# Kernel optimization log

Measured on AMD Instinct MI355X. Metric: run time of the kernel, lower is better.

Reference implementation:

```python
import jax, jax.numpy as jnp
import numpy as np

K = 32
START = K - 2  # index of <START>
STOP = K - 1   # index of <STOP>
NEG = -10000.0
B, T = 512, 2048


def setup_inputs() -> dict:
    key = jax.random.key(0)
    k1, k2, k3, k4 = jax.random.split(key, 4)
    feats = jax.random.normal(k1, (B, T, K), dtype=jnp.float32)
    transitions = jax.random.normal(k2, (K, K), dtype=jnp.float32)
    # constraints set in __init__: never transition TO START, never FROM STOP
    transitions = transitions.at[START, :].set(NEG).at[:, STOP].set(NEG)
    tags = jax.random.randint(k3, (B, T), 0, K - 2)          # real tags only
    lens = jnp.maximum(jax.random.randint(k4, (B,), 0, T), 1)  # at least 1 token
    return {"feats": feats, "transitions": transitions, "tags": tags, "lens": lens}


def _crf_loss(feats, transitions, tags, lens):
    Bn, Tn, Kn = feats.shape
    # ---- forward algorithm (log-partition) ----
    init = jnp.full((Bn, Kn), NEG, feats.dtype).at[:, START].set(0.0)

    def step(alpha, emit):
        # alpha[b,prev] + trans[next,prev] -> logsumexp over prev, then + emit[b,next]
        nxt = jax.scipy.special.logsumexp(
            alpha[:, None, :] + transitions[None, :, :], axis=2) + emit
        return nxt, nxt

    _, alphas = jax.lax.scan(step, init, jnp.swapaxes(feats, 0, 1))  # [T,B,K]
    alphas = jnp.concatenate([init[None], alphas], axis=0)           # [T+1,B,K]
    alpha_at_len = alphas[lens, jnp.arange(Bn)]                      # [B,K]
    forward_score = jax.scipy.special.logsumexp(
        alpha_at_len + transitions[STOP][None, :], axis=1)           # [B]

    # ---- gold score ----
    tags_stop = jnp.where(jnp.arange(Tn)[None, :] < lens[:, None], tags, STOP)
    pad_start = jnp.concatenate(
        [jnp.full((Bn, 1), START, tags.dtype), tags], axis=1)        # [B,T+1]
    pad_stop = jnp.concatenate(
        [tags_stop, jnp.full((Bn, 1), STOP, tags.dtype)], axis=1)    # [B,T+1]
    trans_mask = jnp.arange(Tn + 1)[None, :] <= lens[:, None]        # len+1 transitions
    trans_sc = jnp.where(trans_mask, transitions[pad_stop, pad_start], 0.0).sum(axis=1)
    emit_mask = jnp.arange(Tn)[None, :] < lens[:, None]
    emit_sc = jnp.where(
        emit_mask,
        jnp.take_along_axis(feats, tags[:, :, None], axis=2)[..., 0],
        0.0).sum(axis=1)
    gold_score = trans_sc + emit_sc

    return jnp.mean(forward_score - gold_score)


def reference(feats, transitions, tags, lens):
    return _crf_loss(feats, transitions, tags, lens)
```

## Files before the change

### kernel.cpp

```cpp
#include <hip/hip_runtime.h>
#include <cstdint>
#include <cstddef>

#define Kn 32
#define Bn 512
#define Tn 2048
#define CH 128
#define NC (Tn / CH)
#define GP 4
#define MMB (Bn * (NC / 4))
#define GB  Bn
#define START 30
#define STOP 31
#define LN2F 0.69314718055994530942f
#define QS 16
#define QF (QS * Kn)

typedef __attribute__((ext_vector_type(8))) short bf16x8;
typedef __attribute__((ext_vector_type(16))) float f32x16;
typedef __attribute__((ext_vector_type(2))) float f32x2;

union BF8 { bf16x8 v; unsigned u[4]; };

__device__ __forceinline__ unsigned pk2z(float lo, float hi) {
  return __builtin_amdgcn_perm(__float_as_uint(hi), __float_as_uint(lo),
                               0x07060302u);
}

__device__ __forceinline__ float bcast32(float v, int idx) {
  return __shfl(v, idx, 32);
}

__device__ __forceinline__ void plswap(unsigned& a, unsigned& b) {
  asm("v_permlane32_swap_b32 %0, %1" : "+v"(a), "+v"(b));
}

__global__ __launch_bounds__(256, 6) void crf_fused(
    const float* __restrict__ feats, const float* __restrict__ trans,
    const int* __restrict__ tags, const int* __restrict__ lens,
    float* __restrict__ pmats, float* __restrict__ poffs,
    float* __restrict__ gold_part) {
  __shared__ float lds[4][2][QF];
  const int wid = threadIdx.x >> 6;
  const int lane = threadIdx.x & 63;

  if (blockIdx.x < MMB) {
    const int b = blockIdx.x >> 2;
    const int c = (blockIdx.x & 3) * 4 + wid;
    const int len = lens[b];
    const int nsteps = min(max(len - c * CH, 0), CH);
    if (nsteps == 0) return;

    const int m = lane & 31;
    const int h = lane >> 5;

    f32x2 e1[4], e2[4];
    {
      const float* tr = trans + m * Kn + 8 * h;
#pragma unroll
      for (int j = 0; j < 4; ++j) {
        e1[j] = (f32x2){__expf(tr[2 * j]) * 0.0078125f,
                        __expf(tr[2 * j + 1]) * 0.0078125f};
        e2[j] = (f32x2){__expf(tr[16 + 2 * j]) * 0.0078125f,
                        __expf(tr[16 + 2 * j + 1]) * 0.0078125f};
      }
    }
    unsigned bu[8];
    {
      const int j1 = m - 8 * h;
      const int j2 = m - 16 - 8 * h;
#pragma unroll
      for (int k = 0; k < 4; ++k) {
        bu[k] = (j1 == 2 * k) ? 0x00003F80u
                              : (j1 == 2 * k + 1) ? 0x3F800000u : 0u;
        bu[4 + k] = (j2 == 2 * k) ? 0x00003F80u
                                  : (j2 == 2 * k + 1) ? 0x3F800000u : 0u;
      }
    }
    const f32x16 zf = {0.f, 0.f, 0.f, 0.f, 0.f, 0.f, 0.f, 0.f,
                       0.f, 0.f, 0.f, 0.f, 0.f, 0.f, 0.f, 0.f};
    f32x16 acc;
    float off = 0.0f;

    auto mmstep = [&](float f, bool rn) {
      const float w = __expf(f);
      const f32x2 w2 = {w, w};
      BF8 A1, A2, B1, B2;
#pragma unroll
      for (int j = 0; j < 4; ++j) {
        const f32x2 p1 = e1[j] * w2;
        const f32x2 p2 = e2[j] * w2;
        A1.u[j] = pk2z(p1.x, p1.y);
        A2.u[j] = pk2z(p2.x, p2.y);
        B1.u[j] = bu[j];
        B2.u[j] = bu[4 + j];
      }
      acc = __builtin_amdgcn_mfma_f32_32x32x16_bf16(A2.v, B2.v, zf, 0, 0, 0);
      acc = __builtin_amdgcn_mfma_f32_32x32x16_bf16(A1.v, B1.v, acc, 0, 0, 0);

      if (rn) {
        float mx = acc[0];
#pragma unroll
        for (int r = 1; r < 16; ++r) mx = fmaxf(mx, acc[r]);
#pragma unroll
        for (int d = 1; d < 64; d <<= 1) mx = fmaxf(mx, __shfl_xor(mx, d));
        const int e = (int)((__float_as_uint(mx) >> 23) & 255u);
        const float sc = __uint_as_float((unsigned)(254 - e) << 23);
#pragma unroll
        for (int r = 0; r < 16; ++r) acc[r] *= sc;
        off += (float)(e - 127) * LN2F;
      }

      unsigned qa = pk2z(acc[0], acc[1]);
      unsigned qb = pk2z(acc[2], acc[3]);
      unsigned qc = pk2z(acc[4], acc[5]);
      unsigned qd = pk2z(acc[6], acc[7]);
      unsigned qe = pk2z(acc[8], acc[9]);
      unsigned qf = pk2z(acc[10], acc[11]);
      unsigned qg = pk2z(acc[12], acc[13]);
      unsigned qh = pk2z(acc[14], acc[15]);
      plswap(qa, qc);
      plswap(qb, qd);
      plswap(qe, qg);
      plswap(qf, qh);
      bu[0] = qa; bu[1] = qb; bu[2] = qc; bu[3] = qd;
      bu[4] = qe; bu[5] = qf; bu[6] = qg; bu[7] = qh;
    };

    const float* gsrc = feats + ((size_t)b * Tn + (size_t)c * CH) * Kn;
    float* myl = &lds[wid][0][0];

    {
      float4 v0 = *(const float4*)(gsrc + 0 * 256 + lane * 4);
      float4 v1 = *(const float4*)(gsrc + 1 * 256 + lane * 4);
      *(float4*)(myl + 0 * 256 + lane * 4) = v0;
      *(float4*)(myl + 1 * 256 + lane * 4) = v1;
    }

    const int nq = (nsteps + QS - 1) / QS;
    for (int q = 0; q < nq; ++q) {
      float4 nv0, nv1;
      const bool more = (q + 1 < nq);
      if (more) {
        const float* g = gsrc + (q + 1) * QF + lane * 4;
        nv0 = *(const float4*)(g + 0 * 256);
        nv1 = *(const float4*)(g + 1 * 256);
      }

      const float* lbuf = myl + (q & 1) * QF;
      const int ns = min(QS, nsteps - q * QS);
      const int nb = ns >> 3;
      int tq = 0;
      for (int s8 = 0; s8 < nb; ++s8) {
        float fr[8];
#pragma unroll
        for (int i = 0; i < 8; ++i) fr[i] = lbuf[(tq + i) * Kn + m];
#pragma unroll
        for (int i = 0; i < 8; ++i)
          mmstep(fr[i], ((q * QS + tq + i) & 31) == 31);
        tq += 8;
      }
      const int rem = ns & 7;
      if (rem) {
        float fr[8];
#pragma unroll
        for (int i = 0; i < 8; ++i) fr[i] = lbuf[min(tq + i, QS - 1) * Kn + m];
#pragma unroll
        for (int i = 0; i < 8; ++i)
          if (i < rem) mmstep(fr[i], false);
      }

      if (more) {
        float* nbuf = myl + ((q + 1) & 1) * QF;
        *(float4*)(nbuf + 0 * 256 + lane * 4) = nv0;
        *(float4*)(nbuf + 1 * 256 + lane * 4) = nv1;
      }
    }

    float* pm = pmats + (size_t)(b * NC + c) * (Kn * Kn);
#pragma unroll
    for (int r = 0; r < 16; ++r) {
      const int row = (r & 3) + 8 * (r >> 2) + 4 * h;
      pm[row * Kn + m] = acc[r];
    }
    if (lane == 0) poffs[b * NC + c] = off + 7.0f * LN2F * (float)nsteps;
  } else {
    const int b = blockIdx.x - MMB;
    const int len = lens[b];
    const int* tg = tags + (size_t)b * Tn;
    const float* fbp = feats + (size_t)b * Tn * Kn;
    float acc = 0.f;
    for (int tt = 64 * wid + lane; tt < len; tt += 256) {
      const int tag = tg[tt];
      const int prev = tt ? tg[tt - 1] : START;
      acc += fbp[(size_t)tt * Kn + tag] + trans[tag * Kn + prev];
      if (tt == len - 1) acc += trans[STOP * Kn + tag];
    }
#pragma unroll
    for (int msk = 32; msk >= 1; msk >>= 1) acc += __shfl_xor(acc, msk);
    if (lane == 0) gold_part[b * GP + wid] = acc;
  }
}

__device__ __forceinline__ float renorm_s(float& s, float off) {
  int e = (int)((__float_as_uint(s) >> 23) & 255u);
  e = max(e, __shfl_xor(e, 1));
  e = max(e, __shfl_xor(e, 2));
  e = max(e, __shfl_xor(e, 4));
  e = max(e, __shfl_xor(e, 8));
  e = max(e, __shfl_xor(e, 16));
  s *= __uint_as_float((unsigned)(254 - e) << 23);
  return off + (float)(e - 127) * LN2F;
}

__global__ __launch_bounds__(256, 2) void crf_apply(
    const float* __restrict__ trans, const int* __restrict__ lens,
    const float* __restrict__ pmats, const float* __restrict__ poffs,
    const float* __restrict__ gold_part, float* __restrict__ out) {
  __shared__ float4 smat[NC * 256];
  const int tid = threadIdx.x;
  const int b = blockIdx.x;
  const int len = lens[b];
  const int nc = (len + CH - 1) / CH;

  const float4* gp = (const float4*)(pmats + (size_t)b * NC * (Kn * Kn));
  for (int qq = tid; qq < nc * 256; qq += 256) {
    const int row = (qq >> 3) & 31;
    const int g = qq & 7;
    smat[(qq & ~7) | (g ^ (row & 7))] = gp[qq];
  }
  __syncthreads();
  if (tid >= 64) return;

  const int lane = tid;
  const int n = lane & 31;
  const int hb = (lane >> 5) * 16;
  const int g0 = hb >> 2;
  const int nsw = n & 7;
  float s = (n == START) ? 1.0f : 0.0f;
  float off = 0.0f;
  for (int c = 0; c < nc; ++c) {
    const float4* mr = &smat[(c << 8) | (n << 3)];
    const float4 p0 = mr[(g0 + 0) ^ nsw];
    const float4 p1 = mr[(g0 + 1) ^ nsw];
    const float4 p2 = mr[(g0 + 2) ^ nsw];
    const float4 p3 = mr[(g0 + 3) ^ nsw];
    float a0 = 0.f, a1 = 0.f, a2 = 0.f, a3 = 0.f;
    a0 = fmaf(bcast32(s, hb + 0), p0.x, a0);
    a0 = fmaf(bcast32(s, hb + 1), p0.y, a0);
    a0 = fmaf(bcast32(s, hb + 2), p0.z, a0);
    a0 = fmaf(bcast32(s, hb + 3), p0.w, a0);
    a1 = fmaf(bcast32(s, hb + 4), p1.x, a1);
    a1 = fmaf(bcast32(s, hb + 5), p1.y, a1);
    a1 = fmaf(bcast32(s, hb + 6), p1.z, a1);
    a1 = fmaf(bcast32(s, hb + 7), p1.w, a1);
    a2 = fmaf(bcast32(s, hb + 8), p2.x, a2);
    a2 = fmaf(bcast32(s, hb + 9), p2.y, a2);
    a2 = fmaf(bcast32(s, hb + 10), p2.z, a2);
    a2 = fmaf(bcast32(s, hb + 11), p2.w, a2);
    a3 = fmaf(bcast32(s, hb + 12), p3.x, a3);
    a3 = fmaf(bcast32(s, hb + 13), p3.y, a3);
    a3 = fmaf(bcast32(s, hb + 14), p3.z, a3);
    a3 = fmaf(bcast32(s, hb + 15), p3.w, a3);
    float p = (a0 + a1) + (a2 + a3);
    p += __shfl_xor(p, 32);
    s = p;
    off = renorm_s(s, off);
    off += poffs[b * NC + c];
  }
  const float es = __expf(trans[STOP * Kn + n]);
  float q = s * es;
#pragma unroll
  for (int d = 1; d < 32; d <<= 1) q += __shfl_xor(q, d);
  if (lane == 0) {
    const float fs = __logf(q) + off;
    float gs = 0.f;
#pragma unroll
    for (int gi = 0; gi < GP; ++gi) gs += gold_part[b * GP + gi];
    atomicAdd(out, (fs - gs) * (1.0f / (float)Bn));
  }
}

extern "C" void kernel_launch(void* const* d_in, const int* in_sizes, int n_in,
                              void* d_out, int out_size, void* d_ws, size_t ws_size,
                              hipStream_t stream) {
  const float* feats = (const float*)d_in[0];
  const float* trans = (const float*)d_in[1];
  const int* tags = (const int*)d_in[2];
  const int* lens = (const int*)d_in[3];

  float* gold_part = (float*)d_ws;
  float* poffs = gold_part + (size_t)Bn * GP;
  float* pmats = poffs + (size_t)Bn * NC;

  hipMemsetAsync(d_out, 0, (size_t)out_size * sizeof(float), stream);
  crf_fused<<<MMB + GB, 256, 0, stream>>>(feats, trans, tags, lens, pmats,
                                          poffs, gold_part);
  crf_apply<<<Bn, 256, 0, stream>>>(trans, lens, pmats, poffs, gold_part,
                                    (float*)d_out);
}
```

Measured before the change: 268.3 us.

## Interleave two independent chunk recurrences per wave to hide MFMA latency

Each wave now processes two adjacent time chunks and alternates their dependent MFMA matrix-product steps, so one chain's MFMA latency is covered by the other chain's work. The grid shrinks to two blocks per batch row, the LDS staging buffer is doubled, and launch bounds drop from 6 to 4 waves per SIMD to leave room for the extra registers. In exchange there is less occupancy and fewer blocks, and wave work becomes more uneven when one chunk is shorter than the other.

```diff
diff --git a/kernel.cpp b/kernel.cpp
--- a/kernel.cpp
+++ b/kernel.cpp
@@ -8,7 +8,7 @@
 #define CH 128
 #define NC (Tn / CH)
 #define GP 4
-#define MMB (Bn * (NC / 4))
+#define MMB (Bn * 2)
 #define GB  Bn
 #define START 30
 #define STOP 31
@@ -35,21 +35,23 @@
   asm("v_permlane32_swap_b32 %0, %1" : "+v"(a), "+v"(b));
 }
 
-__global__ __launch_bounds__(256, 6) void crf_fused(
+__global__ __launch_bounds__(256, 4) void crf_fused(
     const float* __restrict__ feats, const float* __restrict__ trans,
     const int* __restrict__ tags, const int* __restrict__ lens,
     float* __restrict__ pmats, float* __restrict__ poffs,
     float* __restrict__ gold_part) {
-  __shared__ float lds[4][2][QF];
+  __shared__ float lds[4][2][2][QF];
   const int wid = threadIdx.x >> 6;
   const int lane = threadIdx.x & 63;
 
   if (blockIdx.x < MMB) {
-    const int b = blockIdx.x >> 2;
-    const int c = (blockIdx.x & 3) * 4 + wid;
+    const int b = blockIdx.x >> 1;
+    const int g = blockIdx.x & 1;
+    const int c0 = 8 * g + 2 * wid;
     const int len = lens[b];
-    const int nsteps = min(max(len - c * CH, 0), CH);
-    if (nsteps == 0) return;
+    const int n0 = min(max(len - c0 * CH, 0), CH);
+    const int n1 = min(max(len - (c0 + 1) * CH, 0), CH);
+    if (n0 == 0) return;
 
     const int m = lane & 31;
     const int h = lane >> 5;
@@ -65,24 +67,27 @@
                         __expf(tr[16 + 2 * j + 1]) * 0.0078125f};
       }
     }
-    unsigned bu[8];
+    unsigned buA[8], buB[8];
     {
       const int j1 = m - 8 * h;
       const int j2 = m - 16 - 8 * h;
 #pragma unroll
       for (int k = 0; k < 4; ++k) {
-        bu[k] = (j1 == 2 * k) ? 0x00003F80u
-                              : (j1 == 2 * k + 1) ? 0x3F800000u : 0u;
-        bu[4 + k] = (j2 == 2 * k) ? 0x00003F80u
-                                  : (j2 == 2 * k + 1) ? 0x3F800000u : 0u;
+        const unsigned v1 = (j1 == 2 * k) ? 0x00003F80u
+                           : (j1 == 2 * k + 1) ? 0x3F800000u : 0u;
+        const unsigned v2 = (j2 == 2 * k) ? 0x00003F80u
+                           : (j2 == 2 * k + 1) ? 0x3F800000u : 0u;
+        buA[k] = v1; buA[4 + k] = v2;
+        buB[k] = v1; buB[4 + k] = v2;
       }
     }
     const f32x16 zf = {0.f, 0.f, 0.f, 0.f, 0.f, 0.f, 0.f, 0.f,
                        0.f, 0.f, 0.f, 0.f, 0.f, 0.f, 0.f, 0.f};
-    f32x16 acc;
-    float off = 0.0f;
-
-    auto mmstep = [&](float f, bool rn) {
+    f32x16 accA, accB;
+    float offA = 0.0f, offB = 0.0f;
+
+    auto mm = [&](unsigned (&bu)[8], f32x16& acc, float& off, float f,
+                  bool rn) {
       const float w = __expf(f);
       const f32x2 w2 = {w, w};
       BF8 A1, A2, B1, B2;
@@ -127,63 +132,110 @@
       bu[4] = qe; bu[5] = qf; bu[6] = qg; bu[7] = qh;
     };
 
-    const float* gsrc = feats + ((size_t)b * Tn + (size_t)c * CH) * Kn;
-    float* myl = &lds[wid][0][0];
+    const float* ga = feats + ((size_t)b * Tn + (size_t)c0 * CH) * Kn;
+    const float* gb = ga + (size_t)CH * Kn;
+    float* myla = &lds[wid][0][0][0];
+    float* mylb = &lds[wid][1][0][0];
 
     {
-      float4 v0 = *(const float4*)(gsrc + 0 * 256 + lane * 4);
-      float4 v1 = *(const float4*)(gsrc + 1 * 256 + lane * 4);
-      *(float4*)(myl + 0 * 256 + lane * 4) = v0;
-      *(float4*)(myl + 1 * 256 + lane * 4) = v1;
-    }
-
-    const int nq = (nsteps + QS - 1) / QS;
+      float4 v0 = *(const float4*)(ga + lane * 4);
+      float4 v1 = *(const float4*)(ga + 256 + lane * 4);
+      *(float4*)(myla + lane * 4) = v0;
+      *(float4*)(myla + 256 + lane * 4) = v1;
+      if (n1) {
+        float4 w0 = *(const float4*)(gb + lane * 4);
+        float4 w1 = *(const float4*)(gb + 256 + lane * 4);
+        *(float4*)(mylb + lane * 4) = w0;
+        *(float4*)(mylb + 256 + lane * 4) = w1;
+      }
+    }
+
+    const int nq = (n0 + QS - 1) / QS;
     for (int q = 0; q < nq; ++q) {
-      float4 nv0, nv1;
-      const bool more = (q + 1 < nq);
-      if (more) {
-        const float* g = gsrc + (q + 1) * QF + lane * 4;
-        nv0 = *(const float4*)(g + 0 * 256);
-        nv1 = *(const float4*)(g + 1 * 256);
-      }
-
-      const float* lbuf = myl + (q & 1) * QF;
-      const int ns = min(QS, nsteps - q * QS);
-      const int nb = ns >> 3;
-      int tq = 0;
-      for (int s8 = 0; s8 < nb; ++s8) {
-        float fr[8];
-#pragma unroll
-        for (int i = 0; i < 8; ++i) fr[i] = lbuf[(tq + i) * Kn + m];
-#pragma unroll
-        for (int i = 0; i < 8; ++i)
-          mmstep(fr[i], ((q * QS + tq + i) & 31) == 31);
-        tq += 8;
-      }
-      const int rem = ns & 7;
-      if (rem) {
-        float fr[8];
-#pragma unroll
-        for (int i = 0; i < 8; ++i) fr[i] = lbuf[min(tq + i, QS - 1) * Kn + m];
-#pragma unroll
-        for (int i = 0; i < 8; ++i)
-          if (i < rem) mmstep(fr[i], false);
-      }
-
-      if (more) {
-        float* nbuf = myl + ((q + 1) & 1) * QF;
-        *(float4*)(nbuf + 0 * 256 + lane * 4) = nv0;
-        *(float4*)(nbuf + 1 * 256 + lane * 4) = nv1;
-      }
-    }
-
-    float* pm = pmats + (size_t)(b * NC + c) * (Kn * Kn);
-#pragma unroll
-    for (int r = 0; r < 16; ++r) {
-      const int row = (r & 3) + 8 * (r >> 2) + 4 * h;
-      pm[row * Kn + m] = acc[r];
-    }
-    if (lane == 0) poffs[b * NC + c] = off + 7.0f * LN2F * (float)nsteps;
+      const bool morea = (q + 1) * QS < n0;
+      const bool moreb = (q + 1) * QS < n1;
+      float4 na0, na1, nb0, nb1;
+      if (morea) {
+        const float* p = ga + (q + 1) * QF + lane * 4;
+        na0 = *(const float4*)(p);
+        na1 = *(const float4*)(p + 256);
+      }
+      if (moreb) {
+        const float* p = gb + (q + 1) * QF + lane * 4;
+        nb0 = *(const float4*)(p);
+        nb1 = *(const float4*)(p + 256);
+      }
+
+      const float* la = myla + (q & 1) * QF;
+      const float* lb = mylb + (q & 1) * QF;
+
+      for (int s8 = 0; s8 < 2; ++s8) {
+        const int base = q * QS + s8 * 8;
+        if (base >= n0) break;
+        const bool rn7 = ((base >> 3) & 3) == 3;
+        float fa[8];
+#pragma unroll
+        for (int i = 0; i < 8; ++i) fa[i] = la[(s8 * 8 + i) * Kn + m];
+
+        if (base + 8 <= n1) {
+          float fb[8];
+#pragma unroll
+          for (int i = 0; i < 8; ++i) fb[i] = lb[(s8 * 8 + i) * Kn + m];
+#pragma unroll
+          for (int i = 0; i < 8; ++i) {
+            mm(buA, accA, offA, fa[i], i == 7 && rn7);
+            mm(buB, accB, offB, fb[i], i == 7 && rn7);
+          }
+        } else if (base < n1) {
+          float fb[8];
+#pragma unroll
+          for (int i = 0; i < 8; ++i) fb[i] = lb[(s8 * 8 + i) * Kn + m];
+#pragma unroll
+          for (int i = 0; i < 8; ++i) {
+            mm(buA, accA, offA, fa[i], i == 7 && rn7);
+            if (base + i < n1) mm(buB, accB, offB, fb[i], false);
+          }
+        } else if (base + 8 <= n0) {
+#pragma unroll
+          for (int i = 0; i < 8; ++i)
+            mm(buA, accA, offA, fa[i], i == 7 && rn7);
+        } else {
+#pragma unroll
+          for (int i = 0; i < 8; ++i)
+            if (base + i < n0) mm(buA, accA, offA, fa[i], false);
+        }
+      }
+
+      if (morea) {
+        float* nb = myla + ((q + 1) & 1) * QF;
+        *(float4*)(nb + lane * 4) = na0;
+        *(float4*)(nb + 256 + lane * 4) = na1;
+      }
+      if (moreb) {
+        float* nb = mylb + ((q + 1) & 1) * QF;
+        *(float4*)(nb + lane * 4) = nb0;
+        *(float4*)(nb + 256 + lane * 4) = nb1;
+      }
+    }
+
+    {
+      float* pm = pmats + (size_t)(b * NC + c0) * (Kn * Kn);
+#pragma unroll
+      for (int r = 0; r < 16; ++r) {
+        const int row = (r & 3) + 8 * (r >> 2) + 4 * h;
+        pm[row * Kn + m] = accA[r];
+      }
+      if (lane == 0) poffs[b * NC + c0] = offA + 7.0f * LN2F * (float)n0;
+    }
+    if (n1) {
+      float* pm = pmats + (size_t)(b * NC + c0 + 1) * (Kn * Kn);
+#pragma unroll
+      for (int r = 0; r < 16; ++r) {
+        const int row = (r & 3) + 8 * (r >> 2) + 4 * h;
+        pm[row * Kn + m] = accB[r];
+      }
+      if (lane == 0) poffs[b * NC + c0 + 1] = offB + 7.0f * LN2F * (float)n1;
+    }
   } else {
     const int b = blockIdx.x - MMB;
     const int len = lens[b];
```

Result: no change. 264.6 us (-1.4%).
